# Optimization experiments

Hardware: AMD Instinct MI355X
Metric: run time of the kernel (lower is better)

## Reference

```python
import jax, jax.numpy as jnp
import numpy as np

N, E, D, O, STEP = 100000, 640000, 128, 64, 10


def setup_inputs() -> dict:
    key = jax.random.key(0)
    k1, k2, k3, k4, k5 = jax.random.split(key, 5)
    x = jax.random.normal(k1, (N, D), dtype=jnp.float32)
    edge_index = jax.random.randint(k2, (2, E), 0, N, dtype=jnp.int64)
    t = jax.random.normal(k3, (STEP, D), dtype=jnp.float32)
    W = jax.random.normal(k4, (O, D), dtype=jnp.float32) * 0.05
    b = jax.random.normal(k5, (O,), dtype=jnp.float32) * 0.05
    return {"x": x, "edge_index": edge_index, "t": t, "W": W, "b": b}


def reference(x, edge_index, t, W, b):
    n = x.shape[0]
    # add self loops
    loops = jnp.arange(n, dtype=edge_index.dtype)
    row = jnp.concatenate([edge_index[0], loops])  # source (x_j)
    col = jnp.concatenate([edge_index[1], loops])  # target (aggregation index)
    # symmetric normalization: deg computed over col (targets)
    deg = jax.ops.segment_sum(jnp.ones_like(row, dtype=x.dtype), col, num_segments=n)
    dinv = deg ** -0.5  # deg >= 1 thanks to self loops
    norm = (dinv[row] * dinv[col])[:, None]  # [E+N, 1]
    # per-channel softmax over the 10 hop weights
    t_norm = jax.nn.softmax(t, axis=0)  # [STEP, D]

    def hop(carry, tk):
        h, y = carry
        h = jax.ops.segment_sum(norm * h[row], col, num_segments=n)  # SpMM hop
        return (h, y + tk * h), None

    (_, y), _ = jax.lax.scan(hop, (x, t_norm[0] * x), t_norm[1:])
    return y @ W.T + b
```

## Files before the change

### kernel.cpp

```cpp
#include <hip/hip_runtime.h>

typedef _Float16 half2_t __attribute__((ext_vector_type(2)));
typedef unsigned int uint;
typedef unsigned long long ull;

#define D 128
#define O 64
#define UNR 8
#define PNW 8
#define MAX_SCAN_BLOCKS 2000
#define ZONE_A 1536
#define ZONE_B 512
#define FILL_BLOCKS 1024

static inline size_t align_up(size_t x, size_t a) { return (x + a - 1) & ~(a - 1); }

__device__ __forceinline__ uint pack_f16(float a, float b) {
  half2_t h;
  h.x = (_Float16)a;
  h.y = (_Float16)b;
  return *(uint*)&h;
}

__device__ __forceinline__ float dot2f(uint a, uint b, float c) {
#if defined(__has_builtin) && __has_builtin(__builtin_amdgcn_fdot2)
  return __builtin_amdgcn_fdot2(*(half2_t*)&a, *(half2_t*)&b, c, false);
#else
  half2_t ha = *(half2_t*)&a, hb = *(half2_t*)&b;
  return c + (float)ha.x * (float)hb.x + (float)ha.y * (float)hb.y;
#endif
}


__global__ __launch_bounds__(256) void setup_k(
    const float* __restrict__ x, uint* __restrict__ h0, int nF4,
    const int* __restrict__ col, int* __restrict__ deg, int E, int n,
    const float* __restrict__ t, float* __restrict__ tn,
    const float* __restrict__ W, uint* __restrict__ Wpk, int step) {
  int bid = blockIdx.x;
  int tid = threadIdx.x;
  if (bid < ZONE_A) {
    int stride = ZONE_A * 256;
    for (int i = bid * 256 + tid; i < nF4; i += stride) {
      float4 v = ((const float4*)x)[i];
      uint2 o;
      o.x = pack_f16(v.x, v.y);
      o.y = pack_f16(v.z, v.w);
      ((uint2*)h0)[i] = o;
    }
  } else if (bid < ZONE_A + ZONE_B) {
    int b = bid - ZONE_A;
    int stride = ZONE_B * 256;
    int nE4 = E >> 2;
    for (int i = b * 256 + tid; i < nE4; i += stride) {
      int4 c = ((const int4*)col)[i];
      if ((unsigned)c.x < (unsigned)n) atomicAdd(&deg[c.x], 1);
      if ((unsigned)c.y < (unsigned)n) atomicAdd(&deg[c.y], 1);
      if ((unsigned)c.z < (unsigned)n) atomicAdd(&deg[c.z], 1);
      if ((unsigned)c.w < (unsigned)n) atomicAdd(&deg[c.w], 1);
    }
    if (b == 0 && tid < (E & 3)) {
      int c = col[(nE4 << 2) + tid];
      if ((unsigned)c < (unsigned)n) atomicAdd(&deg[c], 1);
    }
  } else {
    if (tid < D) {
      float vals[16];
      float m = -1e30f;
      for (int k = 0; k < step; ++k) { vals[k] = t[k * D + tid]; m = fmaxf(m, vals[k]); }
      float ssum = 0.f;
      for (int k = 0; k < step; ++k) { vals[k] = expf(vals[k] - m); ssum += vals[k]; }
      float inv = 1.f / ssum;
      for (int k = 0; k < step; ++k) tn[k * D + tid] = vals[k] * inv;
    }
    for (int i = tid; i < O * 64; i += 256) {
      int o = i & 63, dd = i >> 6;
      Wpk[i] = pack_f16(W[o * D + 2 * dd], W[o * D + 2 * dd + 1]);
    }
  }
}


__global__ __launch_bounds__(256) void scan_all_k(
    const int* __restrict__ deg, int* __restrict__ row_ptr, int* __restrict__ cursor,
    float* __restrict__ dinv, ull* __restrict__ desc, int n) {
  __shared__ int s[256];
  __shared__ int sOff;
  int tid = threadIdx.x, bid = blockIdx.x;
  int gid = bid * 256 + tid;
  int dg = (gid < n) ? deg[gid] : 0;
  if (gid < n) dinv[gid] = rsqrtf((float)(dg + 1));
  s[tid] = dg;
  __syncthreads();
  for (int off = 1; off < 256; off <<= 1) {
    int t = (tid >= off) ? s[tid - off] : 0;
    __syncthreads();
    s[tid] += t;
    __syncthreads();
  }
  if (tid == 0) {
    int agg = s[255];
    ull mine = ((ull)(bid == 0 ? 2u : 1u) << 32) | (uint)agg;
    atomicExch(&desc[bid], mine);
    int off = 0;
    if (bid > 0) {
      int j = bid - 1;
      for (;;) {
        ull d = atomicAdd(&desc[j], 0ULL);
        uint f = (uint)(d >> 32);
        if (f == 0) continue;
        off += (int)(uint)(d & 0xffffffffULL);
        if (f == 2) break;
        --j;
      }
      atomicExch(&desc[bid], ((ull)2u << 32) | (uint)(off + agg));
    }
    sOff = off;
  }
  __syncthreads();
  if (gid < n) {
    int r = s[tid] - dg + sOff;
    row_ptr[gid] = r;
    cursor[gid] = r;
    if (gid == n - 1) row_ptr[n] = r + dg;
  }
}


__global__ void scan1_k(const int* __restrict__ deg, int* __restrict__ row_ptr,
                        int* __restrict__ bsum, float* __restrict__ dinv, int n) {
  __shared__ int s[256];
  int tid = threadIdx.x;
  int gid = blockIdx.x * 256 + tid;
  int dg = (gid < n) ? deg[gid] : 0;
  if (gid < n) dinv[gid] = rsqrtf((float)(dg + 1));
  s[tid] = dg;
  __syncthreads();
  for (int off = 1; off < 256; off <<= 1) {
    int t = (tid >= off) ? s[tid - off] : 0;
    __syncthreads();
    s[tid] += t;
    __syncthreads();
  }
  if (gid < n) row_ptr[gid] = s[tid] - dg;
  if (tid == 255) bsum[blockIdx.x] = s[255];
}

__global__ void scan2_k(int* __restrict__ bsum, int nb) {
  __shared__ int s[512];
  int tid = threadIdx.x;
  int acc = 0;
  for (int base = 0; base < nb; base += 512) {
    int v = (base + tid < nb) ? bsum[base + tid] : 0;
    s[tid] = v;
    __syncthreads();
    for (int off = 1; off < 512; off <<= 1) {
      int t = (tid >= off) ? s[tid - off] : 0;
      __syncthreads();
      s[tid] += t;
      __syncthreads();
    }
    if (base + tid < nb) bsum[base + tid] = s[tid] - v + acc;
    __syncthreads();
    acc += s[511];
    __syncthreads();
  }
}

__global__ void scan3_k(const int* __restrict__ bsum, const int* __restrict__ deg,
                        int* __restrict__ row_ptr, int* __restrict__ cursor, int n) {
  int gid = blockIdx.x * 256 + threadIdx.x;
  if (gid < n) {
    int r = row_ptr[gid] + bsum[blockIdx.x];
    row_ptr[gid] = r;
    cursor[gid] = r;
    if (gid == n - 1) row_ptr[n] = r + deg[gid];
  }
}


__device__ __forceinline__ void fill_one(int u, int v, int n, int* cursor,
                                         const float* dinv, int2* csr) {
  if ((unsigned)v >= (unsigned)n) return;
  if ((unsigned)u >= (unsigned)n) u = 0;
  int slot = atomicAdd(&cursor[v], 1);
  float nrm = dinv[u] * dinv[v];
  csr[slot] = make_int2(u, __float_as_int(nrm));
}

__global__ __launch_bounds__(256) void fill_k(
    const int* __restrict__ rows, const int* __restrict__ cols,
    int* __restrict__ cursor, const float* __restrict__ dinv,
    int2* __restrict__ csr, int E, int n) {
  int stride = gridDim.x * 256;
  int nE4 = E >> 2;
  for (int i = blockIdx.x * 256 + threadIdx.x; i < nE4; i += stride) {
    int4 u4 = ((const int4*)rows)[i];
    int4 v4 = ((const int4*)cols)[i];
    fill_one(u4.x, v4.x, n, cursor, dinv, csr);
    fill_one(u4.y, v4.y, n, cursor, dinv, csr);
    fill_one(u4.z, v4.z, n, cursor, dinv, csr);
    fill_one(u4.w, v4.w, n, cursor, dinv, csr);
  }
  if (blockIdx.x == 0 && threadIdx.x < (E & 3)) {
    int e = (nE4 << 2) + threadIdx.x;
    fill_one(rows[e], cols[e], n, cursor, dinv, csr);
  }
}


template <int DO_Y>
__global__ __launch_bounds__(256) void hop_f_k(
    const uint* __restrict__ h_old, uint* __restrict__ h_new, uint* __restrict__ y,
    const int* __restrict__ row_ptr, const int2* __restrict__ csr,
    const float* __restrict__ dinv, const float* __restrict__ tprev,
    const float* __restrict__ tcur, int n) {
  int wid = (blockIdx.x * blockDim.x + threadIdx.x) >> 6;
  int lane = threadIdx.x & 63;
  if (wid >= n) return;
  int v = __builtin_amdgcn_readfirstlane(wid);
  float dv = dinv[v];
  float ns = dv * dv;
  uint hp = h_old[(size_t)v * 64 + lane];
  half2_t hv = *(half2_t*)&hp;
  float hx = (float)hv.x, hy = (float)hv.y;
  float ax = ns * hx, ay = ns * hy;
  int beg = __builtin_amdgcn_readfirstlane(row_ptr[v]);
  int end = __builtin_amdgcn_readfirstlane(row_ptr[v + 1]);
  for (int i = beg; i < end; i += UNR) {
    int u[UNR];
    float w[UNR];
#pragma unroll
    for (int j = 0; j < UNR; ++j) {
      int ic = i + j;
      int icl = (ic < end - 1) ? ic : (end - 1);
      int2 e = csr[icl];
      u[j] = e.x;
      w[j] = (ic < end) ? __int_as_float(e.y) : 0.f;
    }
    uint g[UNR];
#pragma unroll
    for (int j = 0; j < UNR; ++j) g[j] = h_old[(size_t)u[j] * 64 + lane];
#pragma unroll
    for (int j = 0; j < UNR; ++j) {
      half2_t h = *(half2_t*)&g[j];
      ax += w[j] * (float)h.x;
      ay += w[j] * (float)h.y;
    }
  }
  h_new[(size_t)v * 64 + lane] = pack_f16(ax, ay);
  if (DO_Y) {
    float yx = 0.f, yy = 0.f;
    if (DO_Y != 3) {
      float2 ta = ((const float2*)tprev)[lane];
      yx = ta.x * hx;
      yy = ta.y * hy;
    }
    float2 tb = ((const float2*)tcur)[lane];
    yx += tb.x * ax;
    yy += tb.y * ay;
    if (DO_Y >= 2) {
      uint yo = y[(size_t)v * 64 + lane];
      half2_t yh = *(half2_t*)&yo;
      yx += (float)yh.x;
      yy += (float)yh.y;
    }
    y[(size_t)v * 64 + lane] = pack_f16(yx, yy);
  }
}


__global__ __launch_bounds__(256) void proj_y2_k(
    const uint* __restrict__ y, const uint* __restrict__ Wpk,
    const float* __restrict__ b, float* __restrict__ out, int n) {
  __shared__ uint sy[4][64];
  int tid = threadIdx.x;
  int lane = tid & 63, wv = tid >> 6;
  uint wreg[64];
#pragma unroll
  for (int j = 0; j < 64; ++j) wreg[j] = Wpk[j * 64 + lane];
  float bias = b[lane];
  int wid = (blockIdx.x * blockDim.x + tid) >> 6;
  int vb = wid * PNW;
  int ve = vb + PNW < n ? vb + PNW : n;
  for (int v = vb; v < ve; ++v) {
    sy[wv][lane] = y[(size_t)v * 64 + lane];
    float acc = bias;
#pragma unroll
    for (int q = 0; q < 16; ++q) {
      uint4 yq = *(const uint4*)&sy[wv][q * 4];
      acc = dot2f(yq.x, wreg[q * 4 + 0], acc);
      acc = dot2f(yq.y, wreg[q * 4 + 1], acc);
      acc = dot2f(yq.z, wreg[q * 4 + 2], acc);
      acc = dot2f(yq.w, wreg[q * 4 + 3], acc);
    }
    out[(size_t)v * O + lane] = acc;
  }
}


extern "C" void kernel_launch(void* const* d_in, const int* in_sizes, int n_in,
                              void* d_out, int out_size, void* d_ws, size_t ws_size,
                              hipStream_t stream) {
  const float* x = (const float*)d_in[0];
  const int* ei = (const int*)d_in[1];
  const float* t = (const float*)d_in[2];
  const float* W = (const float*)d_in[3];
  const float* b = (const float*)d_in[4];
  float* out = (float*)d_out;

  int n = in_sizes[0] / D;
  int E = in_sizes[1] / 2;
  int step = in_sizes[2] / D;
  const int* rows = ei;
  const int* cols = ei + E;

  int nb1 = (n + 255) / 256;

  char* p = (char*)d_ws;
  auto alloc = [&](size_t bytes) { char* r = p; p += align_up(bytes, 256); return r; };
  int*   deg     = (int*)alloc((size_t)n * 4);
  ull*   desc    = (ull*)alloc((size_t)nb1 * 8);
  float* dinv    = (float*)alloc((size_t)n * 4);
  int*   row_ptr = (int*)alloc((size_t)(n + 1) * 4);
  int*   cursor  = (int*)alloc((size_t)n * 4);
  int*   bsum    = (int*)alloc(align_up((size_t)nb1 * 4, 256));
  int2*  csr     = (int2*)alloc((size_t)E * 8);
  float* tn      = (float*)alloc((size_t)step * D * 4);
  uint*  Wpk     = (uint*)alloc((size_t)O * 64 * 4);

  size_t NS = (size_t)n * 64;
  uint* h_a  = (uint*)alloc(NS * 4);
  uint* h_b  = (uint*)alloc(NS * 4);
  uint* ybuf = (uint*)alloc(NS * 4);

  size_t zlen = (size_t)((char*)(desc + nb1) - (char*)deg);
  hipMemsetAsync(deg, 0, zlen, stream);

  int nF4 = (int)(NS >> 1);
  setup_k<<<ZONE_A + ZONE_B + 1, 256, 0, stream>>>(x, h_a, nF4, cols, deg, E, n,
                                                   t, tn, W, Wpk, step);

  if (nb1 <= MAX_SCAN_BLOCKS) {
    scan_all_k<<<nb1, 256, 0, stream>>>(deg, row_ptr, cursor, dinv, desc, n);
  } else {
    scan1_k<<<nb1, 256, 0, stream>>>(deg, row_ptr, bsum, dinv, n);
    scan2_k<<<1, 512, 0, stream>>>(bsum, nb1);
    scan3_k<<<nb1, 256, 0, stream>>>(bsum, deg, row_ptr, cursor, n);
  }

  fill_k<<<FILL_BLOCKS, 256, 0, stream>>>(rows, cols, cursor, dinv, csr, E, n);

  int hop_blocks = (n + 3) / 4;
  uint* ho = h_a;
  uint* hn = h_b;
  for (int k = 1; k < step; ++k) {
    const float* tp = tn + (size_t)(k - 1) * D;
    const float* tc = tn + (size_t)k * D;
    if (k & 1) {
      if (k == 1)
        hop_f_k<1><<<hop_blocks, 256, 0, stream>>>(ho, hn, ybuf, row_ptr, csr, dinv, tp, tc, n);
      else
        hop_f_k<2><<<hop_blocks, 256, 0, stream>>>(ho, hn, ybuf, row_ptr, csr, dinv, tp, tc, n);
    } else if (k == step - 1) {
      hop_f_k<3><<<hop_blocks, 256, 0, stream>>>(ho, hn, ybuf, row_ptr, csr, dinv, tp, tc, n);
    } else {
      hop_f_k<0><<<hop_blocks, 256, 0, stream>>>(ho, hn, ybuf, row_ptr, csr, dinv, tp, tc, n);
    }
    uint* tmp = ho; ho = hn; hn = tmp;
  }

  int proj_blocks = (n + PNW * 4 - 1) / (PNW * 4);
  proj_y2_k<<<proj_blocks, 256, 0, stream>>>(ybuf, Wpk, b, out, n);
}
```

Before: 516.2 us.

## Fuse CSR fill into decoupled-lookback scan kernel with per-block readiness flags

Merges the prefix-scan and CSR fill kernels into one launch. Each block publishes a status-3 descriptor once its row_ptr/cursor/dinv values are written, and fill work spin-waits on the descriptors of the source and target blocks before using cursor and dinv. This removes one kernel launch and the global barrier between scan and fill. In exchange it adds spin-waiting, which depends on all ~391 blocks being co-resident to avoid deadlock and adds polling traffic per edge. ZONE_A is also nudged by one.

Measured after the change: 542.6 us. 1.05x slower.

```diff
diff --git a/kernel.cpp b/kernel.cpp
--- a/kernel.cpp
+++ b/kernel.cpp
@@ -9,7 +9,7 @@
 #define UNR 8
 #define PNW 8
 #define MAX_SCAN_BLOCKS 2000
-#define ZONE_A 1536
+#define ZONE_A 1535
 #define ZONE_B 512
 #define FILL_BLOCKS 1024
 
@@ -81,9 +81,23 @@
 }
 
 
-__global__ __launch_bounds__(256) void scan_all_k(
+__device__ __forceinline__ void fill_one_sync(
+    int u, int v, int n, int* __restrict__ cursor, const float* __restrict__ dinv,
+    int2* __restrict__ csr, ull* __restrict__ desc) {
+  if ((unsigned)v >= (unsigned)n) return;
+  if ((unsigned)u >= (unsigned)n) u = 0;
+  while ((uint)(atomicAdd(&desc[v >> 8], 0ULL) >> 32) < 3u) {}
+  while ((uint)(atomicAdd(&desc[u >> 8], 0ULL) >> 32) < 1u) {}
+  int slot = atomicAdd(&cursor[v], 1);
+  float nrm = dinv[u] * dinv[v];
+  csr[slot] = make_int2(u, __float_as_int(nrm));
+}
+
+__global__ __launch_bounds__(256) void scan_fill_k(
     const int* __restrict__ deg, int* __restrict__ row_ptr, int* __restrict__ cursor,
-    float* __restrict__ dinv, ull* __restrict__ desc, int n) {
+    float* __restrict__ dinv, ull* __restrict__ desc,
+    const int* __restrict__ rows, const int* __restrict__ cols,
+    int2* __restrict__ csr, int E, int n) {
   __shared__ int s[256];
   __shared__ int sOff;
   int tid = threadIdx.x, bid = blockIdx.x;
@@ -100,6 +114,7 @@
   }
   if (tid == 0) {
     int agg = s[255];
+    __threadfence();
     ull mine = ((ull)(bid == 0 ? 2u : 1u) << 32) | (uint)agg;
     atomicExch(&desc[bid], mine);
     int off = 0;
@@ -110,7 +125,7 @@
         uint f = (uint)(d >> 32);
         if (f == 0) continue;
         off += (int)(uint)(d & 0xffffffffULL);
-        if (f == 2) break;
+        if (f >= 2) break;
         --j;
       }
       atomicExch(&desc[bid], ((ull)2u << 32) | (uint)(off + agg));
@@ -118,11 +133,33 @@
     sOff = off;
   }
   __syncthreads();
+  int myPrefix = 0;
   if (gid < n) {
     int r = s[tid] - dg + sOff;
     row_ptr[gid] = r;
     cursor[gid] = r;
     if (gid == n - 1) row_ptr[n] = r + dg;
+    if (tid == 255 || gid == n - 1) myPrefix = r + dg;
+  }
+  __syncthreads();
+  if (tid == 0) {
+    __threadfence();
+    atomicExch(&desc[bid], ((ull)3u << 32) | (uint)(sOff + s[255]));
+  }
+
+  int stride = gridDim.x * 256;
+  int nE4 = E >> 2;
+  for (int i = bid * 256 + tid; i < nE4; i += stride) {
+    int4 u4 = ((const int4*)rows)[i];
+    int4 v4 = ((const int4*)cols)[i];
+    fill_one_sync(u4.x, v4.x, n, cursor, dinv, csr, desc);
+    fill_one_sync(u4.y, v4.y, n, cursor, dinv, csr, desc);
+    fill_one_sync(u4.z, v4.z, n, cursor, dinv, csr, desc);
+    fill_one_sync(u4.w, v4.w, n, cursor, dinv, csr, desc);
+  }
+  if (bid == 0 && tid < (E & 3)) {
+    int e = (nE4 << 2) + tid;
+    fill_one_sync(rows[e], cols[e], n, cursor, dinv, csr, desc);
   }
 }
 
@@ -177,7 +214,6 @@
     if (gid == n - 1) row_ptr[n] = r + deg[gid];
   }
 }
-
 
 __device__ __forceinline__ void fill_one(int u, int v, int n, int* cursor,
                                          const float* dinv, int2* csr) {
@@ -342,14 +378,14 @@
                                                    t, tn, W, Wpk, step);
 
   if (nb1 <= MAX_SCAN_BLOCKS) {
-    scan_all_k<<<nb1, 256, 0, stream>>>(deg, row_ptr, cursor, dinv, desc, n);
+    scan_fill_k<<<nb1, 256, 0, stream>>>(deg, row_ptr, cursor, dinv, desc,
+                                         rows, cols, csr, E, n);
   } else {
     scan1_k<<<nb1, 256, 0, stream>>>(deg, row_ptr, bsum, dinv, n);
     scan2_k<<<1, 512, 0, stream>>>(bsum, nb1);
     scan3_k<<<nb1, 256, 0, stream>>>(bsum, deg, row_ptr, cursor, n);
-  }
-
-  fill_k<<<FILL_BLOCKS, 256, 0, stream>>>(rows, cols, cursor, dinv, csr, E, n);
+    fill_k<<<FILL_BLOCKS, 256, 0, stream>>>(rows, cols, cursor, dinv, csr, E, n);
+  }
 
   int hop_blocks = (n + 3) / 4;
   uint* ho = h_a;
```
